# Kernel tuning notes

Hardware: AMD Instinct MI355X
Metric: run time of the kernel (lower is better)

Reference implementation:

```python
import jax, jax.numpy as jnp
import numpy as np

SEQ_LEN = 8192
HEAD_DIM = 128


def setup_inputs() -> dict:
    key = jax.random.key(0)
    kq, kk, kv = jax.random.split(key, 3)
    q = jax.random.normal(kq, (SEQ_LEN, HEAD_DIM), dtype=jnp.float32)
    k = jax.random.normal(kk, (SEQ_LEN, HEAD_DIM), dtype=jnp.float32)
    v = jax.random.normal(kv, (SEQ_LEN, HEAD_DIM), dtype=jnp.float32)
    return {"q": q, "k": k, "v": v}


def reference(q, k, v):
    # FlashAttention computes exact softmax attention; the blocked loops with
    # online max/sum rescaling in the source are an exact reformulation of:
    #   O = softmax(Q K^T) V
    # NOTE: the original module applies no 1/sqrt(d) scaling, so neither do we.
    s = jnp.einsum('nd,md->nm', q, k)          # [N, N] scores
    p = jax.nn.softmax(s, axis=-1)             # stable softmax (online in src)
    return jnp.einsum('nm,md->nd', p, v)       # [N, d]
```

## Files before the change

### kernel.cpp

```cpp
#include <hip/hip_runtime.h>

#define N_SEQ 8192
#define HDIM  128

typedef _Float16 half8v  __attribute__((ext_vector_type(8)));
typedef float    floatx16 __attribute__((ext_vector_type(16)));
typedef unsigned int uint32;

__global__ void prep_kv(const float* __restrict__ K, const float* __restrict__ V,
                        _Float16* __restrict__ K16s, _Float16* __restrict__ Vs) {
    __shared__ float Kl[32 * 132];
    __shared__ float Vl[32 * 132];
    const int t  = threadIdx.x;
    const int nt = blockIdx.x;
    const int n0 = nt * 32;
    #pragma unroll
    for (int kk = 0; kk < 4; kk++) {
        int idx = t + 256 * kk;
        int nl = idx >> 5, c4 = idx & 31;
        float4 f = *(((const float4*)(K + (size_t)(n0 + nl) * HDIM)) + c4);
        float* dk = &Kl[nl * 132 + c4 * 4];
        dk[0] = f.x; dk[1] = f.y; dk[2] = f.z; dk[3] = f.w;
        float4 g = *(((const float4*)(V + (size_t)(n0 + nl) * HDIM)) + c4);
        float* dv = &Vl[nl * 132 + c4 * 4];
        dv[0] = g.x; dv[1] = g.y; dv[2] = g.z; dv[3] = g.w;
    }
    __syncthreads();
    #pragma unroll
    for (int rep = 0; rep < 2; rep++) {
        int ch = t + rep * 256;
        int kc = ch >> 6, lane = ch & 63, l31 = lane & 31, q5 = (lane >> 5) & 1;
        half8v h;
        #pragma unroll
        for (int j = 0; j < 8; j++) h[j] = (_Float16)Kl[l31 * 132 + kc * 16 + q5 * 8 + j];
        *(half8v*)(K16s + (((size_t)nt * 8 + kc) * 64 + lane) * 8) = h;
    }
    #pragma unroll
    for (int rep = 0; rep < 2; rep++) {
        int ch = t + rep * 256;
        int dt = ch >> 7, kc2 = (ch >> 6) & 1, lane = ch & 63, l31 = lane & 31, q5 = (lane >> 5) & 1;
        half8v h;
        #pragma unroll
        for (int j = 0; j < 8; j++) h[j] = (_Float16)Vl[(kc2 * 16 + q5 * 8 + j) * 132 + dt * 32 + l31];
        *(half8v*)(Vs + ((((size_t)nt * 4 + dt) * 2 + kc2) * 64 + lane) * 8) = h;
    }
}

static __device__ __forceinline__ void do_pv(const half8v (&vsrc)[8], const uint32 (&hpk)[8],
                                             floatx16 (&oacc)[4], int q5) {
    #pragma unroll
    for (int kc2 = 0; kc2 < 2; kc2++) {
        uint32 pass0 = q5 ? hpk[4 * kc2 + 0] : hpk[4 * kc2 + 2];
        uint32 pass1 = q5 ? hpk[4 * kc2 + 1] : hpk[4 * kc2 + 3];
        uint32 r0 = (uint32)__shfl_xor((int)pass0, 32, 64);
        uint32 r1 = (uint32)__shfl_xor((int)pass1, 32, 64);
        uint32 b0 = q5 ? r0 : hpk[4 * kc2 + 0];
        uint32 b1 = q5 ? r1 : hpk[4 * kc2 + 1];
        uint32 b2 = q5 ? hpk[4 * kc2 + 2] : r0;
        uint32 b3 = q5 ? hpk[4 * kc2 + 3] : r1;
        uint4 bu = make_uint4(b0, b1, b2, b3);
        half8v bfrag = __builtin_bit_cast(half8v, bu);
        #pragma unroll
        for (int dt = 0; dt < 4; dt++)
            oacc[dt] = __builtin_amdgcn_mfma_f32_32x32x16_f16(vsrc[dt * 2 + kc2], bfrag, oacc[dt], 0, 0, 0);
    }
}

template <bool DO_PV>
static __device__ __forceinline__ void pipe_step(
        const half8v (&qf)[8], half8v (&vin)[8], const half8v (&vprev)[8],
        floatx16 (&oacc)[4], uint32 (&hpk)[8],
        float& runm, float& lsum, float& palpha, bool& pflag,
        const _Float16* __restrict__ K16s, const _Float16* __restrict__ Vs,
        size_t nt, int lane, int q5) {
    half8v kf[8];
    #pragma unroll
    for (int kc = 0; kc < 8; kc++)
        kf[kc] = *(const half8v*)(K16s + ((nt * 8 + kc) * 64 + lane) * 8);
    #pragma unroll
    for (int dt = 0; dt < 4; dt++)
        #pragma unroll
        for (int kc2 = 0; kc2 < 2; kc2++)
            vin[dt * 2 + kc2] = *(const half8v*)(Vs + (((nt * 4 + dt) * 2 + kc2) * 64 + lane) * 8);
    if (pflag) {
        #pragma unroll
        for (int dt = 0; dt < 4; dt++)
            #pragma unroll
            for (int r = 0; r < 16; r++) oacc[dt][r] *= palpha;
        pflag = false;
    }
    if (DO_PV) do_pv(vprev, hpk, oacc, q5);
    floatx16 s0, s1;
    #pragma unroll
    for (int r = 0; r < 16; r++) { s0[r] = 0.0f; s1[r] = 0.0f; }
    #pragma unroll
    for (int kc = 0; kc < 4; kc++)
        s0 = __builtin_amdgcn_mfma_f32_32x32x16_f16(kf[kc], qf[kc], s0, 0, 0, 0);
    #pragma unroll
    for (int kc = 4; kc < 8; kc++)
        s1 = __builtin_amdgcn_mfma_f32_32x32x16_f16(kf[kc], qf[kc], s1, 0, 0, 0);
    float sc[16];
    #pragma unroll
    for (int r = 0; r < 16; r++) sc[r] = s0[r] + s1[r];
    float tm[8];
    #pragma unroll
    for (int r = 0; r < 8; r++) tm[r] = fmaxf(sc[r], sc[r + 8]);
    #pragma unroll
    for (int w = 4; w; w >>= 1)
        #pragma unroll
        for (int r = 0; r < w; r++) tm[r] = fmaxf(tm[r], tm[r + w]);
    float cmax = fmaxf(tm[0], __shfl_xor(tm[0], 32, 64));
    if (__any(cmax > runm + 12.0f)) {
        const float mnew = fmaxf(runm, cmax);
        palpha = __builtin_amdgcn_exp2f(runm - mnew);
        runm = mnew;
        lsum *= palpha;
        pflag = true;
    }
    float p[16];
    #pragma unroll
    for (int r = 0; r < 16; r++) p[r] = __builtin_amdgcn_exp2f(sc[r] - runm);
    float ts[8];
    #pragma unroll
    for (int r = 0; r < 8; r++) ts[r] = p[r] + p[r + 8];
    #pragma unroll
    for (int w = 4; w; w >>= 1)
        #pragma unroll
        for (int r = 0; r < w; r++) ts[r] += ts[r + w];
    lsum += ts[0];
    #pragma unroll
    for (int t2 = 0; t2 < 8; t2++) {
        auto pk = __builtin_amdgcn_cvt_pkrtz(p[2 * t2], p[2 * t2 + 1]);
        hpk[t2] = __builtin_bit_cast(uint32, pk);
    }
}

__launch_bounds__(256, 2)
__global__ void fa_main(const float* __restrict__ Qp, const _Float16* __restrict__ K16s,
                        const _Float16* __restrict__ Vs, float* __restrict__ Opart,
                        float* __restrict__ lpart, float* __restrict__ mpart, int tiles) {
    const int tid  = threadIdx.x;
    const int lane = tid & 63;
    const int wv   = tid >> 6;
    const int l31  = lane & 31;
    const int q5   = lane >> 5;
    const int m0   = blockIdx.x * 128 + wv * 32;
    const int sp   = blockIdx.y;
    const float LOG2E = 1.44269504088896f;

    half8v qf[8];
    {
        const float* qrow = Qp + (size_t)(m0 + l31) * HDIM;
        #pragma unroll
        for (int kc = 0; kc < 8; kc++) {
            const float4 a = *(const float4*)(qrow + kc * 16 + q5 * 8);
            const float4 b = *(const float4*)(qrow + kc * 16 + q5 * 8 + 4);
            half8v h;
            h[0] = (_Float16)(a.x * LOG2E); h[1] = (_Float16)(a.y * LOG2E);
            h[2] = (_Float16)(a.z * LOG2E); h[3] = (_Float16)(a.w * LOG2E);
            h[4] = (_Float16)(b.x * LOG2E); h[5] = (_Float16)(b.y * LOG2E);
            h[6] = (_Float16)(b.z * LOG2E); h[7] = (_Float16)(b.w * LOG2E);
            qf[kc] = h;
        }
    }

    floatx16 oacc[4];
    #pragma unroll
    for (int dt = 0; dt < 4; dt++)
        #pragma unroll
        for (int r = 0; r < 16; r++) oacc[dt][r] = 0.0f;

    float runm = -3.0e38f;
    float lsum = 0.0f;
    float palpha = 0.0f;
    bool  pflag = false;
    uint32 hpk[8];
    half8v va[8], vb[8];

    const size_t nt0 = (size_t)sp * tiles;
    pipe_step<false>(qf, va, va, oacc, hpk, runm, lsum, palpha, pflag, K16s, Vs, nt0, lane, q5);
    for (int p = 0; p < (tiles - 2) / 2; p++) {
        pipe_step<true>(qf, vb, va, oacc, hpk, runm, lsum, palpha, pflag, K16s, Vs, nt0 + 1 + 2 * p, lane, q5);
        pipe_step<true>(qf, va, vb, oacc, hpk, runm, lsum, palpha, pflag, K16s, Vs, nt0 + 2 + 2 * p, lane, q5);
    }
    pipe_step<true>(qf, vb, va, oacc, hpk, runm, lsum, palpha, pflag, K16s, Vs, nt0 + tiles - 1, lane, q5);
    if (pflag) {
        #pragma unroll
        for (int dt = 0; dt < 4; dt++)
            #pragma unroll
            for (int r = 0; r < 16; r++) oacc[dt][r] *= palpha;
    }
    do_pv(vb, hpk, oacc, q5);

    float ltot = lsum + __shfl_xor(lsum, 32, 64);
    if (lane < 32) {
        __builtin_nontemporal_store(ltot, &lpart[(size_t)sp * N_SEQ + m0 + l31]);
        __builtin_nontemporal_store(runm, &mpart[(size_t)sp * N_SEQ + m0 + l31]);
    }
    #pragma unroll
    for (int dt = 0; dt < 4; dt++)
        #pragma unroll
        for (int r = 0; r < 16; r++) {
            int d = dt * 32 + (r & 3) + 8 * (r >> 2) + 4 * q5;
            __builtin_nontemporal_store(oacc[dt][r],
                &Opart[((size_t)sp * HDIM + d) * N_SEQ + m0 + l31]);
        }
}

__global__ void fa_merge(const float* __restrict__ Opart, const float* __restrict__ lpart,
                         const float* __restrict__ mpart, float* __restrict__ Out, int S) {
    __shared__ float lds[64 * 33];
    const int t  = threadIdx.x;
    const int m0 = blockIdx.x * 64;
    const int i  = t & 63;
    const int g  = t >> 6;
    const int m  = m0 + i;
    const int d0 = blockIdx.y * 32 + g * 8;

    float M = -3.0e38f;
    for (int s = 0; s < S; s++) M = fmaxf(M, mpart[(size_t)s * N_SEQ + m]);
    float L = 0.0f;
    for (int s = 0; s < S; s++)
        L += lpart[(size_t)s * N_SEQ + m] * __builtin_amdgcn_exp2f(mpart[(size_t)s * N_SEQ + m] - M);
    const float inv = 1.0f / L;

    float acc[8];
    #pragma unroll
    for (int dd = 0; dd < 8; dd++) acc[dd] = 0.0f;
    for (int s = 0; s < S; s++) {
        const float ww = __builtin_amdgcn_exp2f(mpart[(size_t)s * N_SEQ + m] - M) * inv;
        #pragma unroll
        for (int dd = 0; dd < 8; dd++)
            acc[dd] += __builtin_nontemporal_load(
                &Opart[((size_t)s * HDIM + d0 + dd) * N_SEQ + m]) * ww;
    }
    #pragma unroll
    for (int dd = 0; dd < 8; dd++) lds[i * 33 + g * 8 + dd] = acc[dd];
    __syncthreads();
    const int mi = t >> 2, c = t & 3;
    float4 v0, v1;
    const float* row = &lds[mi * 33 + c * 8];
    v0.x = row[0]; v0.y = row[1]; v0.z = row[2]; v0.w = row[3];
    v1.x = row[4]; v1.y = row[5]; v1.z = row[6]; v1.w = row[7];
    float* outp = Out + (size_t)(m0 + mi) * HDIM + blockIdx.y * 32 + c * 8;
    *(float4*)(outp)     = v0;
    *(float4*)(outp + 4) = v1;
}

__global__ void fa_naive(const float* __restrict__ Q, const float* __restrict__ K,
                         const float* __restrict__ V, float* __restrict__ O) {
    const int m = blockIdx.x;
    const int t = threadIdx.x;
    __shared__ float qs[HDIM];
    __shared__ float ps[256];
    __shared__ float red[256];
    if (t < HDIM) qs[t] = Q[(size_t)m * HDIM + t] * 1.44269504f;
    __syncthreads();
    float om = -3.0e38f, ls = 0.0f, oa = 0.0f;
    for (int nb = 0; nb < N_SEQ; nb += 256) {
        const float* kr = K + (size_t)(nb + t) * HDIM;
        float s = 0.0f;
        #pragma unroll 8
        for (int d = 0; d < HDIM; d++) s += qs[d] * kr[d];
        red[t] = s; __syncthreads();
        for (int st = 128; st > 0; st >>= 1) { if (t < st) red[t] = fmaxf(red[t], red[t + st]); __syncthreads(); }
        float cm = red[0];
        __syncthreads();
        float mn = fmaxf(om, cm);
        float al = __builtin_amdgcn_exp2f(om - mn);
        om = mn;
        float pp = __builtin_amdgcn_exp2f(s - mn);
        ps[t] = pp; red[t] = pp; __syncthreads();
        for (int st = 128; st > 0; st >>= 1) { if (t < st) red[t] += red[t + st]; __syncthreads(); }
        float csum = red[0];
        ls = ls * al + csum;
        if (t < HDIM) {
            float acc = 0.0f;
            for (int j = 0; j < 256; j++) acc += ps[j] * V[(size_t)(nb + j) * HDIM + t];
            oa = oa * al + acc;
        }
        __syncthreads();
    }
    if (t < HDIM) O[(size_t)m * HDIM + t] = oa / ls;
}

extern "C" void kernel_launch(void* const* d_in, const int* in_sizes, int n_in,
                              void* d_out, int out_size, void* d_ws, size_t ws_size,
                              hipStream_t stream) {
    const float* q = (const float*)d_in[0];
    const float* k = (const float*)d_in[1];
    const float* v = (const float*)d_in[2];
    float* out = (float*)d_out;

    const size_t MB = 1024ull * 1024ull;
    int S = 0;
    for (int s = 8; s >= 1; s >>= 1) {
        size_t need = 4 * MB + (size_t)s * (4 * MB + 64 * 1024);
        if (ws_size >= need) { S = s; break; }
    }
    if (S == 0) {
        fa_naive<<<N_SEQ, 256, 0, stream>>>(q, k, v, out);
        return;
    }
    char* ws = (char*)d_ws;
    _Float16* K16s = (_Float16*)ws;
    _Float16* Vs   = (_Float16*)(ws + 2 * MB);
    float* Opart   = (float*)(ws + 4 * MB);
    float* lpart   = (float*)(ws + 4 * MB + (size_t)S * 4 * MB);
    float* mpart   = lpart + (size_t)S * N_SEQ;

    prep_kv<<<dim3(N_SEQ / 32), dim3(256), 0, stream>>>(k, v, K16s, Vs);
    fa_main<<<dim3(N_SEQ / 128, S), dim3(256), 0, stream>>>(q, K16s, Vs, Opart, lpart, mpart, (N_SEQ / 32) / S);
    fa_merge<<<dim3(N_SEQ / 64, HDIM / 32), dim3(256), 0, stream>>>(Opart, lpart, mpart, out, S);
}
```

Baseline: 126.7 us.

## Split KV range across wave pairs within block and combine partials in LDS

Each block now handles 64 query rows instead of 128, and its four waves form two pairs. Each pair processes half of the block's KV split, and the partial outputs and softmax stats are merged through shared memory before the global store. Launch bounds rise to 4 blocks per CU to raise occupancy, and twice as many blocks are launched. The cost is LDS usage, a block barrier, and register pressure under the tighter launch bound, which may cause spills.

```diff
diff --git a/kernel.cpp b/kernel.cpp
--- a/kernel.cpp
+++ b/kernel.cpp
@@ -135,16 +135,19 @@
     }
 }
 
-__launch_bounds__(256, 2)
+__launch_bounds__(256, 4)
 __global__ void fa_main(const float* __restrict__ Qp, const _Float16* __restrict__ K16s,
                         const _Float16* __restrict__ Vs, float* __restrict__ Opart,
-                        float* __restrict__ lpart, float* __restrict__ mpart, int tiles) {
+                        float* __restrict__ lpart, float* __restrict__ mpart, int tilesPerHalf) {
+    __shared__ float comb[2][64][65];
+    __shared__ float mlm[2][32], mll[2][32];
     const int tid  = threadIdx.x;
     const int lane = tid & 63;
     const int wv   = tid >> 6;
     const int l31  = lane & 31;
     const int q5   = lane >> 5;
-    const int m0   = blockIdx.x * 128 + wv * 32;
+    const int kh   = wv >> 1;
+    const int m0   = blockIdx.x * 64 + (wv & 1) * 32;
     const int sp   = blockIdx.y;
     const float LOG2E = 1.44269504088896f;
 
@@ -177,13 +180,13 @@
     uint32 hpk[8];
     half8v va[8], vb[8];
 
-    const size_t nt0 = (size_t)sp * tiles;
+    const size_t nt0 = (size_t)sp * (2 * tilesPerHalf) + (size_t)kh * tilesPerHalf;
     pipe_step<false>(qf, va, va, oacc, hpk, runm, lsum, palpha, pflag, K16s, Vs, nt0, lane, q5);
-    for (int p = 0; p < (tiles - 2) / 2; p++) {
+    for (int p = 0; p < (tilesPerHalf - 2) / 2; p++) {
         pipe_step<true>(qf, vb, va, oacc, hpk, runm, lsum, palpha, pflag, K16s, Vs, nt0 + 1 + 2 * p, lane, q5);
         pipe_step<true>(qf, va, vb, oacc, hpk, runm, lsum, palpha, pflag, K16s, Vs, nt0 + 2 + 2 * p, lane, q5);
     }
-    pipe_step<true>(qf, vb, va, oacc, hpk, runm, lsum, palpha, pflag, K16s, Vs, nt0 + tiles - 1, lane, q5);
+    pipe_step<true>(qf, vb, va, oacc, hpk, runm, lsum, palpha, pflag, K16s, Vs, nt0 + tilesPerHalf - 1, lane, q5);
     if (pflag) {
         #pragma unroll
         for (int dt = 0; dt < 4; dt++)
@@ -193,18 +196,35 @@
     do_pv(vb, hpk, oacc, q5);
 
     float ltot = lsum + __shfl_xor(lsum, 32, 64);
-    if (lane < 32) {
-        __builtin_nontemporal_store(ltot, &lpart[(size_t)sp * N_SEQ + m0 + l31]);
-        __builtin_nontemporal_store(runm, &mpart[(size_t)sp * N_SEQ + m0 + l31]);
-    }
-    #pragma unroll
-    for (int dt = 0; dt < 4; dt++)
-        #pragma unroll
-        for (int r = 0; r < 16; r++) {
-            int d = dt * 32 + (r & 3) + 8 * (r >> 2) + 4 * q5;
-            __builtin_nontemporal_store(oacc[dt][r],
-                &Opart[((size_t)sp * HDIM + d) * N_SEQ + m0 + l31]);
+    if (wv >= 2) {
+        #pragma unroll
+        for (int dt = 0; dt < 4; dt++)
+            #pragma unroll
+            for (int r = 0; r < 16; r++) comb[wv - 2][lane][dt * 16 + r] = oacc[dt][r];
+        if (lane < 32) { mlm[wv - 2][l31] = runm; mll[wv - 2][l31] = ltot; }
+    }
+    __syncthreads();
+    if (wv < 2) {
+        const float mb = mlm[wv][l31];
+        const float lb = mll[wv][l31];
+        const float M  = fmaxf(runm, mb);
+        const float aa = __builtin_amdgcn_exp2f(runm - M);
+        const float ab = __builtin_amdgcn_exp2f(mb - M);
+        const float lt = ltot * aa + lb * ab;
+        if (lane < 32) {
+            __builtin_nontemporal_store(lt, &lpart[(size_t)sp * N_SEQ + m0 + l31]);
+            __builtin_nontemporal_store(M,  &mpart[(size_t)sp * N_SEQ + m0 + l31]);
         }
+        #pragma unroll
+        for (int dt = 0; dt < 4; dt++)
+            #pragma unroll
+            for (int r = 0; r < 16; r++) {
+                int d = dt * 32 + (r & 3) + 8 * (r >> 2) + 4 * q5;
+                float val = oacc[dt][r] * aa + comb[wv][lane][dt * 16 + r] * ab;
+                __builtin_nontemporal_store(val,
+                    &Opart[((size_t)sp * HDIM + d) * N_SEQ + m0 + l31]);
+            }
+    }
 }
 
 __global__ void fa_merge(const float* __restrict__ Opart, const float* __restrict__ lpart,
@@ -294,7 +314,7 @@
 
     const size_t MB = 1024ull * 1024ull;
     int S = 0;
-    for (int s = 8; s >= 1; s >>= 1) {
+    for (int s = 8; s >= 2; s >>= 1) {
         size_t need = 4 * MB + (size_t)s * (4 * MB + 64 * 1024);
         if (ws_size >= need) { S = s; break; }
     }
@@ -310,6 +330,6 @@
     float* mpart   = lpart + (size_t)S * N_SEQ;
 
     prep_kv<<<dim3(N_SEQ / 32), dim3(256), 0, stream>>>(k, v, K16s, Vs);
-    fa_main<<<dim3(N_SEQ / 128, S), dim3(256), 0, stream>>>(q, K16s, Vs, Opart, lpart, mpart, (N_SEQ / 32) / S);
+    fa_main<<<dim3(N_SEQ / 64, S), dim3(256), 0, stream>>>(q, K16s, Vs, Opart, lpart, mpart, (N_SEQ / 32) / S / 2);
     fa_merge<<<dim3(N_SEQ / 64, HDIM / 32), dim3(256), 0, stream>>>(Opart, lpart, mpart, out, S);
 }
```

Result: slower. 329.0 us (+159.6%).

## Stage K/V tiles through a shared LDS triple buffer via global_load_lds

Applied to the files above, without the earlier changes.

Previously each of the four waves in a block loaded the same fp16 K and V tile from global memory straight into its own registers. Now the waves cooperatively copy each tile into a three-slot LDS ring using direct global-to-LDS loads. The next tile is prefetched while the current one is computed, and the K and V fragments are read back from LDS. This cuts the block's global/L2 traffic for K/V by the number of waves. In exchange it adds a block-wide barrier per tile, 48KB of LDS per block, and extra LDS read traffic.

```diff
diff --git a/kernel.cpp b/kernel.cpp
--- a/kernel.cpp
+++ b/kernel.cpp
@@ -43,6 +43,22 @@
         #pragma unroll
         for (int j = 0; j < 8; j++) h[j] = (_Float16)Vl[(kc2 * 16 + q5 * 8 + j) * 132 + dt * 32 + l31];
         *(half8v*)(Vs + ((((size_t)nt * 4 + dt) * 2 + kc2) * 64 + lane) * 8) = h;
+    }
+}
+
+static __device__ __forceinline__ void stage_tile(
+        const char* __restrict__ K16s, const char* __restrict__ Vs,
+        char* lds_raw, int buf, size_t nt, int wv, int lane) {
+    #pragma unroll
+    for (int k2 = 0; k2 < 4; k2++) {
+        const int ch = wv * 4 + k2;
+        const char* g = (ch < 8)
+            ? K16s + ((nt * 8 + ch) * 64 + lane) * 16
+            : Vs   + ((nt * 8 + (ch - 8)) * 64 + lane) * 16;
+        char* l = lds_raw + ((size_t)buf * 16 + ch) * 1024;
+        __builtin_amdgcn_global_load_lds(
+            (const __attribute__((address_space(1))) void*)g,
+            (__attribute__((address_space(3))) void*)l, 16, 0, 0);
     }
 }
 
@@ -66,79 +82,11 @@
     }
 }
 
-template <bool DO_PV>
-static __device__ __forceinline__ void pipe_step(
-        const half8v (&qf)[8], half8v (&vin)[8], const half8v (&vprev)[8],
-        floatx16 (&oacc)[4], uint32 (&hpk)[8],
-        float& runm, float& lsum, float& palpha, bool& pflag,
-        const _Float16* __restrict__ K16s, const _Float16* __restrict__ Vs,
-        size_t nt, int lane, int q5) {
-    half8v kf[8];
-    #pragma unroll
-    for (int kc = 0; kc < 8; kc++)
-        kf[kc] = *(const half8v*)(K16s + ((nt * 8 + kc) * 64 + lane) * 8);
-    #pragma unroll
-    for (int dt = 0; dt < 4; dt++)
-        #pragma unroll
-        for (int kc2 = 0; kc2 < 2; kc2++)
-            vin[dt * 2 + kc2] = *(const half8v*)(Vs + (((nt * 4 + dt) * 2 + kc2) * 64 + lane) * 8);
-    if (pflag) {
-        #pragma unroll
-        for (int dt = 0; dt < 4; dt++)
-            #pragma unroll
-            for (int r = 0; r < 16; r++) oacc[dt][r] *= palpha;
-        pflag = false;
-    }
-    if (DO_PV) do_pv(vprev, hpk, oacc, q5);
-    floatx16 s0, s1;
-    #pragma unroll
-    for (int r = 0; r < 16; r++) { s0[r] = 0.0f; s1[r] = 0.0f; }
-    #pragma unroll
-    for (int kc = 0; kc < 4; kc++)
-        s0 = __builtin_amdgcn_mfma_f32_32x32x16_f16(kf[kc], qf[kc], s0, 0, 0, 0);
-    #pragma unroll
-    for (int kc = 4; kc < 8; kc++)
-        s1 = __builtin_amdgcn_mfma_f32_32x32x16_f16(kf[kc], qf[kc], s1, 0, 0, 0);
-    float sc[16];
-    #pragma unroll
-    for (int r = 0; r < 16; r++) sc[r] = s0[r] + s1[r];
-    float tm[8];
-    #pragma unroll
-    for (int r = 0; r < 8; r++) tm[r] = fmaxf(sc[r], sc[r + 8]);
-    #pragma unroll
-    for (int w = 4; w; w >>= 1)
-        #pragma unroll
-        for (int r = 0; r < w; r++) tm[r] = fmaxf(tm[r], tm[r + w]);
-    float cmax = fmaxf(tm[0], __shfl_xor(tm[0], 32, 64));
-    if (__any(cmax > runm + 12.0f)) {
-        const float mnew = fmaxf(runm, cmax);
-        palpha = __builtin_amdgcn_exp2f(runm - mnew);
-        runm = mnew;
-        lsum *= palpha;
-        pflag = true;
-    }
-    float p[16];
-    #pragma unroll
-    for (int r = 0; r < 16; r++) p[r] = __builtin_amdgcn_exp2f(sc[r] - runm);
-    float ts[8];
-    #pragma unroll
-    for (int r = 0; r < 8; r++) ts[r] = p[r] + p[r + 8];
-    #pragma unroll
-    for (int w = 4; w; w >>= 1)
-        #pragma unroll
-        for (int r = 0; r < w; r++) ts[r] += ts[r + w];
-    lsum += ts[0];
-    #pragma unroll
-    for (int t2 = 0; t2 < 8; t2++) {
-        auto pk = __builtin_amdgcn_cvt_pkrtz(p[2 * t2], p[2 * t2 + 1]);
-        hpk[t2] = __builtin_bit_cast(uint32, pk);
-    }
-}
-
 __launch_bounds__(256, 2)
 __global__ void fa_main(const float* __restrict__ Qp, const _Float16* __restrict__ K16s,
                         const _Float16* __restrict__ Vs, float* __restrict__ Opart,
                         float* __restrict__ lpart, float* __restrict__ mpart, int tiles) {
+    __shared__ __align__(16) char lds_raw[3 * 16 * 1024];
     const int tid  = threadIdx.x;
     const int lane = tid & 63;
     const int wv   = tid >> 6;
@@ -147,6 +95,11 @@
     const int m0   = blockIdx.x * 128 + wv * 32;
     const int sp   = blockIdx.y;
     const float LOG2E = 1.44269504088896f;
+    const char* K16b = (const char*)K16s;
+    const char* Vsb  = (const char*)Vs;
+
+    const size_t nt0 = (size_t)sp * tiles;
+    stage_tile(K16b, Vsb, lds_raw, 0, nt0, wv, lane);
 
     half8v qf[8];
     {
@@ -175,22 +128,91 @@
     float palpha = 0.0f;
     bool  pflag = false;
     uint32 hpk[8];
-    half8v va[8], vb[8];
-
-    const size_t nt0 = (size_t)sp * tiles;
-    pipe_step<false>(qf, va, va, oacc, hpk, runm, lsum, palpha, pflag, K16s, Vs, nt0, lane, q5);
-    for (int p = 0; p < (tiles - 2) / 2; p++) {
-        pipe_step<true>(qf, vb, va, oacc, hpk, runm, lsum, palpha, pflag, K16s, Vs, nt0 + 1 + 2 * p, lane, q5);
-        pipe_step<true>(qf, va, vb, oacc, hpk, runm, lsum, palpha, pflag, K16s, Vs, nt0 + 2 + 2 * p, lane, q5);
-    }
-    pipe_step<true>(qf, vb, va, oacc, hpk, runm, lsum, palpha, pflag, K16s, Vs, nt0 + tiles - 1, lane, q5);
-    if (pflag) {
-        #pragma unroll
-        for (int dt = 0; dt < 4; dt++)
+
+    int bc = 0, bn = 1, bp = 2;
+    for (int t = 0; t < tiles; ++t) {
+        __syncthreads();
+        if (t + 1 < tiles)
+            stage_tile(K16b, Vsb, lds_raw, bn, nt0 + t + 1, wv, lane);
+        if (t > 0) {
+            half8v vf[8];
+            const char* bpb = lds_raw + (size_t)bp * 16 * 1024 + 8 * 1024 + lane * 16;
             #pragma unroll
-            for (int r = 0; r < 16; r++) oacc[dt][r] *= palpha;
-    }
-    do_pv(vb, hpk, oacc, q5);
+            for (int vc = 0; vc < 8; vc++)
+                vf[vc] = *(const half8v*)(bpb + vc * 1024);
+            if (pflag) {
+                #pragma unroll
+                for (int dt = 0; dt < 4; dt++)
+                    #pragma unroll
+                    for (int r = 0; r < 16; r++) oacc[dt][r] *= palpha;
+                pflag = false;
+            }
+            do_pv(vf, hpk, oacc, q5);
+        }
+        half8v kf[8];
+        const char* bcb = lds_raw + (size_t)bc * 16 * 1024 + lane * 16;
+        #pragma unroll
+        for (int kc = 0; kc < 8; kc++)
+            kf[kc] = *(const half8v*)(bcb + kc * 1024);
+        floatx16 s0, s1;
+        #pragma unroll
+        for (int r = 0; r < 16; r++) { s0[r] = 0.0f; s1[r] = 0.0f; }
+        #pragma unroll
+        for (int kc = 0; kc < 4; kc++)
+            s0 = __builtin_amdgcn_mfma_f32_32x32x16_f16(kf[kc], qf[kc], s0, 0, 0, 0);
+        #pragma unroll
+        for (int kc = 4; kc < 8; kc++)
+            s1 = __builtin_amdgcn_mfma_f32_32x32x16_f16(kf[kc], qf[kc], s1, 0, 0, 0);
+        float sc[16];
+        #pragma unroll
+        for (int r = 0; r < 16; r++) sc[r] = s0[r] + s1[r];
+        float tm[8];
+        #pragma unroll
+        for (int r = 0; r < 8; r++) tm[r] = fmaxf(sc[r], sc[r + 8]);
+        #pragma unroll
+        for (int w = 4; w; w >>= 1)
+            #pragma unroll
+            for (int r = 0; r < w; r++) tm[r] = fmaxf(tm[r], tm[r + w]);
+        float cmax = fmaxf(tm[0], __shfl_xor(tm[0], 32, 64));
+        if (__any(cmax > runm + 12.0f)) {
+            const float mnew = fmaxf(runm, cmax);
+            palpha = __builtin_amdgcn_exp2f(runm - mnew);
+            runm = mnew;
+            lsum *= palpha;
+            pflag = true;
+        }
+        float p[16];
+        #pragma unroll
+        for (int r = 0; r < 16; r++) p[r] = __builtin_amdgcn_exp2f(sc[r] - runm);
+        float ts[8];
+        #pragma unroll
+        for (int r = 0; r < 8; r++) ts[r] = p[r] + p[r + 8];
+        #pragma unroll
+        for (int w = 4; w; w >>= 1)
+            #pragma unroll
+            for (int r = 0; r < w; r++) ts[r] += ts[r + w];
+        lsum += ts[0];
+        #pragma unroll
+        for (int t2 = 0; t2 < 8; t2++) {
+            auto pk = __builtin_amdgcn_cvt_pkrtz(p[2 * t2], p[2 * t2 + 1]);
+            hpk[t2] = __builtin_bit_cast(uint32, pk);
+        }
+        int tmpb = bp; bp = bc; bc = bn; bn = tmpb;
+    }
+    {
+        half8v vf[8];
+        const char* bpb = lds_raw + (size_t)bp * 16 * 1024 + 8 * 1024 + lane * 16;
+        #pragma unroll
+        for (int vc = 0; vc < 8; vc++)
+            vf[vc] = *(const half8v*)(bpb + vc * 1024);
+        if (pflag) {
+            #pragma unroll
+            for (int dt = 0; dt < 4; dt++)
+                #pragma unroll
+                for (int r = 0; r < 16; r++) oacc[dt][r] *= palpha;
+        }
+        do_pv(vf, hpk, oacc, q5);
+    }
 
     float ltot = lsum + __shfl_xor(lsum, 32, 64);
     if (lane < 32) {
```

Measured after the change: 128.5 us. About the same (+1.4%).
